# Kernel optimization log

Measured on AMD Instinct MI355X. Metric: run time of the kernel, lower is better.

The kernel has to match this reference:

```python
import jax, jax.numpy as jnp
import numpy as np

N = 100000      # nodes
E = 1600000     # edges (avg degree 16)
F_IN = 128      # num_node_features
H = 64          # hidden_features
C = 40          # num_classes


def _glorot(key, shape):
    lim = np.sqrt(6.0 / (shape[0] + shape[1]))
    return jax.random.uniform(key, shape, jnp.float32, -lim, lim)


def setup_inputs() -> dict:
    key = jax.random.key(0)
    k = jax.random.split(key, 4)
    x = jax.random.normal(k[0], (N, F_IN), dtype=jnp.float32)
    edge_index = jax.random.randint(k[1], (2, E), 0, N, dtype=jnp.int32)
    W1 = _glorot(k[2], (F_IN, H))
    b1 = jnp.zeros((H,), jnp.float32)
    W2 = _glorot(k[3], (H, C))
    b2 = jnp.zeros((C,), jnp.float32)
    return {"x": x, "edge_index": edge_index, "W1": W1, "b1": b1, "W2": W2, "b2": b2}


def _gcn_conv(x, src, dst, dinv_sqrt, W, b):
    # GCNConv: out = D^{-1/2} (A + I) D^{-1/2} (x W) + b
    h = x @ W                                        # [N, out]
    norm = dinv_sqrt[src] * dinv_sqrt[dst]           # [E+N]
    msg = h[src] * norm[:, None]                     # gather + scale
    agg = jax.ops.segment_sum(msg, dst, num_segments=N)
    return agg + b


def reference(x, edge_index, W1, b1, W2, b2):
    loop = jnp.arange(N, dtype=edge_index.dtype)
    src = jnp.concatenate([edge_index[0], loop])     # add self-loops
    dst = jnp.concatenate([edge_index[1], loop])
    # degree of A + I (counts in-edges at destination, incl. self-loop)
    deg = jax.ops.segment_sum(jnp.ones_like(dst, jnp.float32), dst, num_segments=N)
    dinv_sqrt = jax.lax.rsqrt(deg)                   # deg >= 1 due to self-loops

    h = _gcn_conv(x, src, dst, dinv_sqrt, W1, b1)
    h = jax.nn.relu(h)
    # F.dropout(training=self.training) is identity in eval mode
    out = _gcn_conv(h, src, dst, dinv_sqrt, W2, b2)
    return out
```

## Files before the change

kernel.cpp:

```cpp
#include <hip/hip_runtime.h>
#include <hip/hip_fp16.h>
#include <cstdint>
#include <cstddef>

#define NPB_SHIFT 8
#define NPB (1 << NPB_SHIFT)
#define CHUNK 4096
#define BCHUNK 8192

typedef _Float16 half8_t __attribute__((ext_vector_type(8)));
typedef _Float16 half4_t __attribute__((ext_vector_type(4)));
typedef float floatx4 __attribute__((ext_vector_type(4)));

__device__ inline float ush2f(unsigned short u) {
  __half_raw r; r.x = u;
  return __half2float(__half(r));
}
__device__ inline void h8f(uint4 v, float* f) {
  f[0] = ush2f((unsigned short)(v.x & 0xffff)); f[1] = ush2f((unsigned short)(v.x >> 16));
  f[2] = ush2f((unsigned short)(v.y & 0xffff)); f[3] = ush2f((unsigned short)(v.y >> 16));
  f[4] = ush2f((unsigned short)(v.z & 0xffff)); f[5] = ush2f((unsigned short)(v.z >> 16));
  f[6] = ush2f((unsigned short)(v.w & 0xffff)); f[7] = ush2f((unsigned short)(v.w >> 16));
}


__global__ void k_zero_i32(int* __restrict__ p, int n) {
  int i = blockIdx.x * blockDim.x + threadIdx.x;
  if (i < n) p[i] = 0;
}

__global__ __launch_bounds__(256) void k_bcount(const int* __restrict__ dst,
                                                int* __restrict__ btot, int E, int nbuck) {
  __shared__ int cnt[512];
  int tid = threadIdx.x;
  for (int i = tid; i < nbuck; i += 256) cnt[i] = 0;
  __syncthreads();
  int base = blockIdx.x * BCHUNK;
  int end = min(base + BCHUNK, E);
  for (int e = base + tid; e < end; e += 256) atomicAdd(&cnt[dst[e] >> NPB_SHIFT], 1);
  __syncthreads();
  for (int i = tid; i < nbuck; i += 256)
    if (cnt[i]) atomicAdd(&btot[i], cnt[i]);
}

__global__ void k_bscan(const int* __restrict__ btot, int* __restrict__ bbase,
                        int* __restrict__ bfill, int nbuck, int E) {
  __shared__ int tmp[512];
  int tid = threadIdx.x;
  int v = (tid < nbuck) ? btot[tid] : 0;
  tmp[tid] = v;
  __syncthreads();
  for (int off = 1; off < 512; off <<= 1) {
    int t = (tid >= off) ? tmp[tid - off] : 0;
    __syncthreads();
    tmp[tid] += t;
    __syncthreads();
  }
  if (tid < nbuck) { int ex = tmp[tid] - v; bbase[tid] = ex; bfill[tid] = ex; }
  if (tid == 0) bbase[nbuck] = E;
}

__global__ __launch_bounds__(256) void k_partition(const int* __restrict__ src,
                                                   const int* __restrict__ dst,
                                                   int* __restrict__ bfill,
                                                   unsigned* __restrict__ tmp,
                                                   int E, int nbuck) {
  __shared__ int cnt[512];
  __shared__ int base[512];
  __shared__ int cur[512];
  int tid = threadIdx.x;
  int cbase = blockIdx.x * CHUNK;
  for (int i = tid; i < nbuck; i += 256) { cnt[i] = 0; cur[i] = 0; }
  __syncthreads();
  int s[16], d[16];
  bool valid[16];
#pragma unroll
  for (int u = 0; u < 16; ++u) {
    int e = cbase + u * 256 + tid;
    valid[u] = e < E;
    s[u] = valid[u] ? src[e] : 0;
    d[u] = valid[u] ? dst[e] : 0;
    if (valid[u]) atomicAdd(&cnt[d[u] >> NPB_SHIFT], 1);
  }
  __syncthreads();
  for (int i = tid; i < nbuck; i += 256)
    if (cnt[i]) base[i] = atomicAdd(&bfill[i], cnt[i]);
  __syncthreads();
#pragma unroll
  for (int u = 0; u < 16; ++u) {
    if (valid[u]) {
      int b = d[u] >> NPB_SHIFT;
      int r = atomicAdd(&cur[b], 1);
      tmp[base[b] + r] = ((unsigned)s[u] << NPB_SHIFT) | (unsigned)(d[u] & (NPB - 1));
    }
  }
}

__global__ __launch_bounds__(256) void k_csr_count(const unsigned* __restrict__ tmp,
                                                   const int* __restrict__ bbase,
                                                   float* __restrict__ dinv,
                                                   int* __restrict__ offset,
                                                   int N, int E, int nbuck) {
  __shared__ int cnt[NPB];
  __shared__ int scan[NPB];
  int b = blockIdx.x, tid = threadIdx.x;
  int nbase = b << NPB_SHIFT;
  int nloc = min(NPB, N - nbase);
  cnt[tid] = 0;
  __syncthreads();
  int ebeg = bbase[b], eend = bbase[b + 1];
  for (int j = ebeg + tid; j < eend; j += 256) atomicAdd(&cnt[tmp[j] & (NPB - 1)], 1);
  __syncthreads();
  int v = cnt[tid];
  scan[tid] = v;
  __syncthreads();
  for (int off = 1; off < NPB; off <<= 1) {
    int t = (tid >= off) ? scan[tid - off] : 0;
    __syncthreads();
    scan[tid] += t;
    __syncthreads();
  }
  if (tid < nloc) {
    offset[nbase + tid] = ebeg + scan[tid] - v;
    dinv[nbase + tid] = rsqrtf((float)(v + 1));
  }
  if (b == nbuck - 1 && tid == 0) offset[N] = E;
}

__global__ __launch_bounds__(256) void k_csr2(const unsigned* __restrict__ tmp,
                                              const int* __restrict__ offset,
                                              const float* __restrict__ dinv,
                                              int2* __restrict__ sedge, int N) {
  __shared__ int fillL[NPB];
  __shared__ float dloc[NPB];
  int b = blockIdx.x;
  int nbase = b << NPB_SHIFT;
  int nend = min(nbase + NPB, N);
  int nloc = nend - nbase;
  int tid = threadIdx.x;
  for (int i = tid; i < nloc; i += 256) {
    fillL[i] = offset[nbase + i];
    dloc[i] = dinv[nbase + i];
  }
  __syncthreads();
  int ebeg = offset[nbase];
  int eend = offset[nend];
  int j = ebeg + tid;
  for (; j + 3 * 256 < eend; j += 4 * 256) {
    unsigned p[4];
#pragma unroll
    for (int u = 0; u < 4; ++u) p[u] = tmp[j + u * 256];
    float dv[4];
#pragma unroll
    for (int u = 0; u < 4; ++u) dv[u] = dinv[p[u] >> NPB_SHIFT];
#pragma unroll
    for (int u = 0; u < 4; ++u) {
      int dl = p[u] & (NPB - 1);
      int pos = atomicAdd(&fillL[dl], 1);
      sedge[pos] = make_int2((int)(p[u] >> NPB_SHIFT), __float_as_int(dv[u] * dloc[dl]));
    }
  }
  for (; j < eend; j += 256) {
    unsigned p = tmp[j];
    int dl = p & (NPB - 1);
    int s = (int)(p >> NPB_SHIFT);
    int pos = atomicAdd(&fillL[dl], 1);
    sedge[pos] = make_int2(s, __float_as_int(dinv[s] * dloc[dl]));
  }
}

template <int K, int COLS, int MT, int KC, int OS>
__global__ __launch_bounds__(256) void k_gemm_mfma(const float* __restrict__ x,
                                                   const float* __restrict__ W,
                                                   _Float16* __restrict__ out, int n) {
  int lane = threadIdx.x & 63;
  int quad = lane >> 4;
  int l15 = lane & 15;
  int gwave = (blockIdx.x * blockDim.x + threadIdx.x) >> 6;
  int nwave = (gridDim.x * blockDim.x) >> 6;
  int ntiles = (n + 15) >> 4;

  half8_t afrag[MT][KC];
#pragma unroll
  for (int m = 0; m < MT; ++m) {
    int colw = m * 16 + l15;
    if (colw > COLS - 1) colw = COLS - 1;
#pragma unroll
    for (int c = 0; c < KC; ++c) {
#pragma unroll
      for (int j = 0; j < 8; ++j) {
        int kk = c * 32 + quad * 8 + j;
        afrag[m][c][j] = (_Float16)W[kk * COLS + colw];
      }
    }
  }

  for (int tile = gwave; tile < ntiles; tile += nwave) {
    int node0 = tile << 4;
    int nodeB = node0 + l15;
    int nodeC = nodeB < n ? nodeB : n - 1;
    const float* xr = x + (size_t)nodeC * K;
    half8_t bfrag[KC];
#pragma unroll
    for (int c = 0; c < KC; ++c) {
      float4 lo = *(const float4*)(xr + c * 32 + quad * 8);
      float4 hi = *(const float4*)(xr + c * 32 + quad * 8 + 4);
      bfrag[c][0] = (_Float16)lo.x; bfrag[c][1] = (_Float16)lo.y;
      bfrag[c][2] = (_Float16)lo.z; bfrag[c][3] = (_Float16)lo.w;
      bfrag[c][4] = (_Float16)hi.x; bfrag[c][5] = (_Float16)hi.y;
      bfrag[c][6] = (_Float16)hi.z; bfrag[c][7] = (_Float16)hi.w;
    }
    floatx4 acc[MT];
#pragma unroll
    for (int m = 0; m < MT; ++m) acc[m] = (floatx4){0.f, 0.f, 0.f, 0.f};
#pragma unroll
    for (int c = 0; c < KC; ++c)
#pragma unroll
      for (int m = 0; m < MT; ++m)
        acc[m] = __builtin_amdgcn_mfma_f32_16x16x32_f16(afrag[m][c], bfrag[c], acc[m], 0, 0, 0);

    if (nodeB < n) {
#pragma unroll
      for (int m = 0; m < MT; ++m) {
        int colBase = m * 16 + quad * 4;
        if (colBase < OS) {
          half4_t hv = {(_Float16)acc[m][0], (_Float16)acc[m][1],
                        (_Float16)acc[m][2], (_Float16)acc[m][3]};
          *(half4_t*)(out + (size_t)nodeB * OS + colBase) = hv;
        }
      }
    }
  }
}

template <int F, int S8, bool RELU>
__global__ __launch_bounds__(256) void k_agg_v8(const uint4* __restrict__ h8,
                                                const int* __restrict__ offset,
                                                const int2* __restrict__ sedge,
                                                const float* __restrict__ dinv,
                                                const float* __restrict__ bias,
                                                float* __restrict__ outp, int n) {
  constexpr int F8 = F / 8;
  int lane = threadIdx.x & 63;
  int g = lane >> 3;
  int t = lane & 7;
  int node = (blockIdx.x * blockDim.x + threadIdx.x) >> 6;
  if (node >= n) return;
  bool tv = t < F8;
  float di = dinv[node];
  float acc[8];
#pragma unroll
  for (int i = 0; i < 8; ++i) acc[i] = 0.f;

  if (g == 0 && tv) {
    float v[8];
    h8f(h8[(size_t)node * S8 + t], v);
    float s = di * di;
#pragma unroll
    for (int i = 0; i < 8; ++i) acc[i] = v[i] * s;
  }

  int beg = offset[node], end = offset[node + 1];
  int j = beg;
  for (; j + 16 <= end; j += 16) {
    int2 eA = sedge[j + g];
    int2 eB = sedge[j + 8 + g];
    uint4 rA = tv ? h8[(size_t)eA.x * S8 + t] : make_uint4(0, 0, 0, 0);
    uint4 rB = tv ? h8[(size_t)eB.x * S8 + t] : make_uint4(0, 0, 0, 0);
    float vA[8], vB[8];
    h8f(rA, vA); h8f(rB, vB);
    float nA = __int_as_float(eA.y), nB = __int_as_float(eB.y);
#pragma unroll
    for (int i = 0; i < 8; ++i) acc[i] = fmaf(vA[i], nA, acc[i]);
#pragma unroll
    for (int i = 0; i < 8; ++i) acc[i] = fmaf(vB[i], nB, acc[i]);
  }
  for (; j + 8 <= end; j += 8) {
    int2 e = sedge[j + g];
    uint4 rv = tv ? h8[(size_t)e.x * S8 + t] : make_uint4(0, 0, 0, 0);
    float v[8];
    h8f(rv, v);
    float nm = __int_as_float(e.y);
#pragma unroll
    for (int i = 0; i < 8; ++i) acc[i] = fmaf(v[i], nm, acc[i]);
  }
  for (; j < end; j += 8) {
    int r = end - j;
    int gi = (g < r) ? g : (r - 1);
    int2 e = sedge[j + gi];
    float nm = (g < r) ? __int_as_float(e.y) : 0.f;
    uint4 rv = tv ? h8[(size_t)e.x * S8 + t] : make_uint4(0, 0, 0, 0);
    float v[8];
    h8f(rv, v);
#pragma unroll
    for (int i = 0; i < 8; ++i) acc[i] = fmaf(v[i], nm, acc[i]);
  }

#pragma unroll
  for (int i = 0; i < 8; ++i) acc[i] += __shfl_xor(acc[i], 8);
#pragma unroll
  for (int i = 0; i < 8; ++i) acc[i] += __shfl_xor(acc[i], 16);
#pragma unroll
  for (int i = 0; i < 8; ++i) acc[i] += __shfl_xor(acc[i], 32);

  if (lane < F8) {
    const float* bb = bias + lane * 8;
    float4 r0 = make_float4(acc[0] + bb[0], acc[1] + bb[1], acc[2] + bb[2], acc[3] + bb[3]);
    float4 r1 = make_float4(acc[4] + bb[4], acc[5] + bb[5], acc[6] + bb[6], acc[7] + bb[7]);
    if (RELU) {
      r0.x = fmaxf(r0.x, 0.f); r0.y = fmaxf(r0.y, 0.f);
      r0.z = fmaxf(r0.z, 0.f); r0.w = fmaxf(r0.w, 0.f);
      r1.x = fmaxf(r1.x, 0.f); r1.y = fmaxf(r1.y, 0.f);
      r1.z = fmaxf(r1.z, 0.f); r1.w = fmaxf(r1.w, 0.f);
    }
    float4* o4 = (float4*)(outp + (size_t)node * F + lane * 8);
    o4[0] = r0; o4[1] = r1;
  }
}


extern "C" void kernel_launch(void* const* d_in, const int* in_sizes, int n_in,
                              void* d_out, int out_size, void* d_ws, size_t ws_size,
                              hipStream_t stream) {
  const float* x  = (const float*)d_in[0];
  const int*   ei = (const int*)d_in[1];
  const float* W1 = (const float*)d_in[2];
  const float* b1 = (const float*)d_in[3];
  const float* W2 = (const float*)d_in[4];
  const float* b2 = (const float*)d_in[5];
  float* out = (float*)d_out;

  const int F_IN = 128, HID = 64, C = 40, CPAD = 48;
  int N = in_sizes[0] / F_IN;
  int E = in_sizes[1] / 2;
  const int* src = ei;
  const int* dst = ei + E;
  int nbuck = (N + NPB - 1) >> NPB_SHIFT;

  char* w = (char*)d_ws;
  size_t o = 0;
  auto alloc = [&](size_t bytes) -> void* {
    void* p = w + o;
    o = (o + bytes + 255) & ~(size_t)255;
    return p;
  };
  float*    dinv   = (float*)alloc((size_t)N * 4);
  int*      offset = (int*)alloc((size_t)(N + 1) * 4);
  int*      btot   = (int*)alloc(512 * 4);
  int*      bbase  = (int*)alloc(513 * 4);
  int*      bfill  = (int*)alloc(512 * 4);
  unsigned* tmp    = (unsigned*)alloc((size_t)E * 4);
  int2*     sedge  = (int2*)alloc((size_t)E * 8);
  _Float16* h      = (_Float16*)alloc((size_t)N * HID * 2);
  float*    h1     = (float*)alloc((size_t)N * HID * 4);
  _Float16* h2     = (_Float16*)alloc((size_t)N * CPAD * 2);

  dim3 b256(256);

  k_zero_i32<<<dim3(2), b256, 0, stream>>>(btot, 512);
  k_bcount<<<dim3((E + BCHUNK - 1) / BCHUNK), b256, 0, stream>>>(dst, btot, E, nbuck);
  k_bscan<<<dim3(1), dim3(512), 0, stream>>>(btot, bbase, bfill, nbuck, E);

  k_partition<<<dim3((E + CHUNK - 1) / CHUNK), b256, 0, stream>>>(src, dst, bfill, tmp, E, nbuck);
  k_csr_count<<<dim3(nbuck), b256, 0, stream>>>(tmp, bbase, dinv, offset, N, E, nbuck);
  k_csr2<<<dim3(nbuck), b256, 0, stream>>>(tmp, offset, dinv, sedge, N);

  k_gemm_mfma<128, 64, 4, 4, 64><<<dim3(256), b256, 0, stream>>>(x, W1, h, N);
  k_agg_v8<64, 8, true><<<dim3((N + 3) / 4), b256, 0, stream>>>(
      (const uint4*)h, offset, sedge, dinv, b1, h1, N);

  k_gemm_mfma<64, 40, 3, 2, 48><<<dim3(256), b256, 0, stream>>>(h1, W2, h2, N);
  k_agg_v8<40, 6, false><<<dim3((N + 3) / 4), b256, 0, stream>>>(
      (const uint4*)h2, offset, sedge, dinv, b2, out, N);
}
```

Measured before the change: 284.9 us.

## Fold source normalization into GEMM output and drop per-edge norm storage

Pre-scales each GEMM output row by dinv[src], so aggregation only sums gathered rows and applies dinv[dst] once at the end. The per-edge weight is no longer needed, so the CSR stores only 4-byte source indices instead of int2, and the two CSR kernels merge into one. The layer-2 intermediate drops its padding from 48 to 40 columns, and the zero kernel becomes a memset. This cuts edge-array bandwidth, per-edge FMAs and one launch, at the cost of a slightly different fp16 rounding order.

```diff
diff --git a/kernel.cpp b/kernel.cpp
--- a/kernel.cpp
+++ b/kernel.cpp
@@ -23,11 +23,6 @@
   f[6] = ush2f((unsigned short)(v.w & 0xffff)); f[7] = ush2f((unsigned short)(v.w >> 16));
 }
 
-
-__global__ void k_zero_i32(int* __restrict__ p, int n) {
-  int i = blockIdx.x * blockDim.x + threadIdx.x;
-  if (i < n) p[i] = 0;
-}
 
 __global__ __launch_bounds__(256) void k_bcount(const int* __restrict__ dst,
                                                 int* __restrict__ btot, int E, int nbuck) {
@@ -96,13 +91,15 @@
   }
 }
 
-__global__ __launch_bounds__(256) void k_csr_count(const unsigned* __restrict__ tmp,
+__global__ __launch_bounds__(256) void k_csr_build(const unsigned* __restrict__ tmp,
                                                    const int* __restrict__ bbase,
                                                    float* __restrict__ dinv,
                                                    int* __restrict__ offset,
+                                                   int* __restrict__ ssrc,
                                                    int N, int E, int nbuck) {
   __shared__ int cnt[NPB];
   __shared__ int scan[NPB];
+  __shared__ int fillL[NPB];
   int b = blockIdx.x, tid = threadIdx.x;
   int nbase = b << NPB_SHIFT;
   int nloc = min(NPB, N - nbase);
@@ -120,58 +117,36 @@
     scan[tid] += t;
     __syncthreads();
   }
+  int myoff = ebeg + scan[tid] - v;
+  fillL[tid] = myoff;
   if (tid < nloc) {
-    offset[nbase + tid] = ebeg + scan[tid] - v;
+    offset[nbase + tid] = myoff;
     dinv[nbase + tid] = rsqrtf((float)(v + 1));
   }
   if (b == nbuck - 1 && tid == 0) offset[N] = E;
-}
-
-__global__ __launch_bounds__(256) void k_csr2(const unsigned* __restrict__ tmp,
-                                              const int* __restrict__ offset,
-                                              const float* __restrict__ dinv,
-                                              int2* __restrict__ sedge, int N) {
-  __shared__ int fillL[NPB];
-  __shared__ float dloc[NPB];
-  int b = blockIdx.x;
-  int nbase = b << NPB_SHIFT;
-  int nend = min(nbase + NPB, N);
-  int nloc = nend - nbase;
-  int tid = threadIdx.x;
-  for (int i = tid; i < nloc; i += 256) {
-    fillL[i] = offset[nbase + i];
-    dloc[i] = dinv[nbase + i];
-  }
-  __syncthreads();
-  int ebeg = offset[nbase];
-  int eend = offset[nend];
+  __syncthreads();
   int j = ebeg + tid;
   for (; j + 3 * 256 < eend; j += 4 * 256) {
     unsigned p[4];
 #pragma unroll
     for (int u = 0; u < 4; ++u) p[u] = tmp[j + u * 256];
-    float dv[4];
-#pragma unroll
-    for (int u = 0; u < 4; ++u) dv[u] = dinv[p[u] >> NPB_SHIFT];
 #pragma unroll
     for (int u = 0; u < 4; ++u) {
-      int dl = p[u] & (NPB - 1);
-      int pos = atomicAdd(&fillL[dl], 1);
-      sedge[pos] = make_int2((int)(p[u] >> NPB_SHIFT), __float_as_int(dv[u] * dloc[dl]));
+      int pos = atomicAdd(&fillL[p[u] & (NPB - 1)], 1);
+      ssrc[pos] = (int)(p[u] >> NPB_SHIFT);
     }
   }
   for (; j < eend; j += 256) {
     unsigned p = tmp[j];
-    int dl = p & (NPB - 1);
-    int s = (int)(p >> NPB_SHIFT);
-    int pos = atomicAdd(&fillL[dl], 1);
-    sedge[pos] = make_int2(s, __float_as_int(dinv[s] * dloc[dl]));
+    int pos = atomicAdd(&fillL[p & (NPB - 1)], 1);
+    ssrc[pos] = (int)(p >> NPB_SHIFT);
   }
 }
 
 template <int K, int COLS, int MT, int KC, int OS>
 __global__ __launch_bounds__(256) void k_gemm_mfma(const float* __restrict__ x,
                                                    const float* __restrict__ W,
+                                                   const float* __restrict__ dinv,
                                                    _Float16* __restrict__ out, int n) {
   int lane = threadIdx.x & 63;
   int quad = lane >> 4;
@@ -200,6 +175,7 @@
     int nodeB = node0 + l15;
     int nodeC = nodeB < n ? nodeB : n - 1;
     const float* xr = x + (size_t)nodeC * K;
+    float dv = dinv[nodeC];
     half8_t bfrag[KC];
 #pragma unroll
     for (int c = 0; c < KC; ++c) {
@@ -223,9 +199,9 @@
 #pragma unroll
       for (int m = 0; m < MT; ++m) {
         int colBase = m * 16 + quad * 4;
-        if (colBase < OS) {
-          half4_t hv = {(_Float16)acc[m][0], (_Float16)acc[m][1],
-                        (_Float16)acc[m][2], (_Float16)acc[m][3]};
+        if (colBase < COLS) {
+          half4_t hv = {(_Float16)(acc[m][0] * dv), (_Float16)(acc[m][1] * dv),
+                        (_Float16)(acc[m][2] * dv), (_Float16)(acc[m][3] * dv)};
           *(half4_t*)(out + (size_t)nodeB * OS + colBase) = hv;
         }
       }
@@ -236,7 +212,7 @@
 template <int F, int S8, bool RELU>
 __global__ __launch_bounds__(256) void k_agg_v8(const uint4* __restrict__ h8,
                                                 const int* __restrict__ offset,
-                                                const int2* __restrict__ sedge,
+                                                const int* __restrict__ ssrc,
                                                 const float* __restrict__ dinv,
                                                 const float* __restrict__ bias,
                                                 float* __restrict__ outp, int n) {
@@ -255,45 +231,39 @@
   if (g == 0 && tv) {
     float v[8];
     h8f(h8[(size_t)node * S8 + t], v);
-    float s = di * di;
-#pragma unroll
-    for (int i = 0; i < 8; ++i) acc[i] = v[i] * s;
+#pragma unroll
+    for (int i = 0; i < 8; ++i) acc[i] = v[i];
   }
 
   int beg = offset[node], end = offset[node + 1];
   int j = beg;
   for (; j + 16 <= end; j += 16) {
-    int2 eA = sedge[j + g];
-    int2 eB = sedge[j + 8 + g];
-    uint4 rA = tv ? h8[(size_t)eA.x * S8 + t] : make_uint4(0, 0, 0, 0);
-    uint4 rB = tv ? h8[(size_t)eB.x * S8 + t] : make_uint4(0, 0, 0, 0);
+    int sA = ssrc[j + g];
+    int sB = ssrc[j + 8 + g];
+    uint4 rA = tv ? h8[(size_t)sA * S8 + t] : make_uint4(0, 0, 0, 0);
+    uint4 rB = tv ? h8[(size_t)sB * S8 + t] : make_uint4(0, 0, 0, 0);
     float vA[8], vB[8];
     h8f(rA, vA); h8f(rB, vB);
-    float nA = __int_as_float(eA.y), nB = __int_as_float(eB.y);
-#pragma unroll
-    for (int i = 0; i < 8; ++i) acc[i] = fmaf(vA[i], nA, acc[i]);
-#pragma unroll
-    for (int i = 0; i < 8; ++i) acc[i] = fmaf(vB[i], nB, acc[i]);
+#pragma unroll
+    for (int i = 0; i < 8; ++i) acc[i] += vA[i] + vB[i];
   }
   for (; j + 8 <= end; j += 8) {
-    int2 e = sedge[j + g];
-    uint4 rv = tv ? h8[(size_t)e.x * S8 + t] : make_uint4(0, 0, 0, 0);
+    int s = ssrc[j + g];
+    uint4 rv = tv ? h8[(size_t)s * S8 + t] : make_uint4(0, 0, 0, 0);
     float v[8];
     h8f(rv, v);
-    float nm = __int_as_float(e.y);
-#pragma unroll
-    for (int i = 0; i < 8; ++i) acc[i] = fmaf(v[i], nm, acc[i]);
-  }
-  for (; j < end; j += 8) {
+#pragma unroll
+    for (int i = 0; i < 8; ++i) acc[i] += v[i];
+  }
+  if (j < end) {
     int r = end - j;
     int gi = (g < r) ? g : (r - 1);
-    int2 e = sedge[j + gi];
-    float nm = (g < r) ? __int_as_float(e.y) : 0.f;
-    uint4 rv = tv ? h8[(size_t)e.x * S8 + t] : make_uint4(0, 0, 0, 0);
+    int s = ssrc[j + gi];
+    uint4 rv = (tv && g < r) ? h8[(size_t)s * S8 + t] : make_uint4(0, 0, 0, 0);
     float v[8];
     h8f(rv, v);
 #pragma unroll
-    for (int i = 0; i < 8; ++i) acc[i] = fmaf(v[i], nm, acc[i]);
+    for (int i = 0; i < 8; ++i) acc[i] += v[i];
   }
 
 #pragma unroll
@@ -305,8 +275,10 @@
 
   if (lane < F8) {
     const float* bb = bias + lane * 8;
-    float4 r0 = make_float4(acc[0] + bb[0], acc[1] + bb[1], acc[2] + bb[2], acc[3] + bb[3]);
-    float4 r1 = make_float4(acc[4] + bb[4], acc[5] + bb[5], acc[6] + bb[6], acc[7] + bb[7]);
+    float4 r0 = make_float4(fmaf(acc[0], di, bb[0]), fmaf(acc[1], di, bb[1]),
+                            fmaf(acc[2], di, bb[2]), fmaf(acc[3], di, bb[3]));
+    float4 r1 = make_float4(fmaf(acc[4], di, bb[4]), fmaf(acc[5], di, bb[5]),
+                            fmaf(acc[6], di, bb[6]), fmaf(acc[7], di, bb[7]));
     if (RELU) {
       r0.x = fmaxf(r0.x, 0.f); r0.y = fmaxf(r0.y, 0.f);
       r0.z = fmaxf(r0.z, 0.f); r0.w = fmaxf(r0.w, 0.f);
@@ -330,7 +302,7 @@
   const float* b2 = (const float*)d_in[5];
   float* out = (float*)d_out;
 
-  const int F_IN = 128, HID = 64, C = 40, CPAD = 48;
+  const int F_IN = 128, HID = 64, C = 40;
   int N = in_sizes[0] / F_IN;
   int E = in_sizes[1] / 2;
   const int* src = ei;
@@ -350,26 +322,25 @@
   int*      bbase  = (int*)alloc(513 * 4);
   int*      bfill  = (int*)alloc(512 * 4);
   unsigned* tmp    = (unsigned*)alloc((size_t)E * 4);
-  int2*     sedge  = (int2*)alloc((size_t)E * 8);
-  _Float16* h      = (_Float16*)alloc((size_t)N * HID * 2);
+  int*      ssrc   = (int*)alloc((size_t)E * 4);
+  _Float16* g1     = (_Float16*)alloc((size_t)N * HID * 2);
   float*    h1     = (float*)alloc((size_t)N * HID * 4);
-  _Float16* h2     = (_Float16*)alloc((size_t)N * CPAD * 2);
+  _Float16* g2     = (_Float16*)alloc((size_t)N * C * 2);
 
   dim3 b256(256);
 
-  k_zero_i32<<<dim3(2), b256, 0, stream>>>(btot, 512);
+  hipMemsetAsync(btot, 0, 512 * 4, stream);
   k_bcount<<<dim3((E + BCHUNK - 1) / BCHUNK), b256, 0, stream>>>(dst, btot, E, nbuck);
   k_bscan<<<dim3(1), dim3(512), 0, stream>>>(btot, bbase, bfill, nbuck, E);
 
   k_partition<<<dim3((E + CHUNK - 1) / CHUNK), b256, 0, stream>>>(src, dst, bfill, tmp, E, nbuck);
-  k_csr_count<<<dim3(nbuck), b256, 0, stream>>>(tmp, bbase, dinv, offset, N, E, nbuck);
-  k_csr2<<<dim3(nbuck), b256, 0, stream>>>(tmp, offset, dinv, sedge, N);
-
-  k_gemm_mfma<128, 64, 4, 4, 64><<<dim3(256), b256, 0, stream>>>(x, W1, h, N);
+  k_csr_build<<<dim3(nbuck), b256, 0, stream>>>(tmp, bbase, dinv, offset, ssrc, N, E, nbuck);
+
+  k_gemm_mfma<128, 64, 4, 4, 64><<<dim3(256), b256, 0, stream>>>(x, W1, dinv, g1, N);
   k_agg_v8<64, 8, true><<<dim3((N + 3) / 4), b256, 0, stream>>>(
-      (const uint4*)h, offset, sedge, dinv, b1, h1, N);
-
-  k_gemm_mfma<64, 40, 3, 2, 48><<<dim3(256), b256, 0, stream>>>(h1, W2, h2, N);
-  k_agg_v8<40, 6, false><<<dim3((N + 3) / 4), b256, 0, stream>>>(
-      (const uint4*)h2, offset, sedge, dinv, b2, out, N);
-}
+      (const uint4*)g1, offset, ssrc, dinv, b1, h1, N);
+
+  k_gemm_mfma<64, 40, 3, 2, 40><<<dim3(256), b256, 0, stream>>>(h1, W2, dinv, g2, N);
+  k_agg_v8<40, 5, false><<<dim3((N + 3) / 4), b256, 0, stream>>>(
+      (const uint4*)g2, offset, ssrc, dinv, b2, out, N);
+}
```

Result: faster. 269.7 us (-5.3%).
